# Kernel optimization log

Measured on AMD Instinct MI355X. Metric: run time of the kernel, lower is better.

## Reference

```python
import jax, jax.numpy as jnp
import numpy as np

NUM_HEADS = 12


def setup_inputs() -> dict:
    key = jax.random.key(0)
    k1, k2, k3 = jax.random.split(key, 3)
    B, S, D = 2, 2048, 768
    x = jax.random.normal(k1, (B, S, D), dtype=jnp.float32)
    # torch Linear init: normal(std=0.002) weights, zero bias; stored as [in, out]
    W_qkv = jax.random.normal(k2, (D, 3 * D), dtype=jnp.float32) * 0.002
    b_qkv = jnp.zeros((3 * D,), dtype=jnp.float32)
    W_vw = jax.random.normal(k3, (D, D), dtype=jnp.float32) * 0.002
    b_vw = jnp.zeros((D,), dtype=jnp.float32)
    mask = jnp.ones((B, S), dtype=jnp.int32)  # padding mask, all valid
    return {"x": x, "W_qkv": W_qkv, "b_qkv": b_qkv, "W_vw": W_vw, "b_vw": b_vw, "mask": mask}


def reference(x, W_qkv, b_qkv, W_vw, b_vw, mask):
    B, S, D = x.shape
    H = NUM_HEADS
    Dh = D // H
    qkv = (x @ W_qkv + b_qkv).reshape(B, S, 3, H, Dh)
    q, k, v = qkv[:, :, 0], qkv[:, :, 1], qkv[:, :, 2]
    # [B, H, S, S] attention scores (full matrix, as in original)
    w = jnp.einsum('bshd,bzhd->bhsz', q, k)
    w = w / jnp.sqrt(jnp.asarray(Dh, dtype=x.dtype))  # scale=True
    # log-mask trick: padding mask [B,1,1,S] * causal tril [1,1,S,S]
    causal = jnp.tril(jnp.ones((S, S), dtype=x.dtype))
    wholemask = mask.astype(x.dtype)[:, None, None, :] * causal[None, None]
    w = w + jnp.log(wholemask)
    w = jax.nn.softmax(w, axis=-1)
    vw = jnp.einsum('bhsz,bzhd->bshd', w, v).reshape(B, S, D)
    return vw @ W_vw + b_vw
```

## Files before the change

kernel.cpp:

```cpp
#include <hip/hip_runtime.h>
#include <hip/hip_bf16.h>
#include <cmath>
#include <cstddef>

#define B_    2
#define S_    2048
#define D_    768
#define H_    12
#define DH_   64
#define NQKV_ 2304

typedef __attribute__((ext_vector_type(8))) short  short8;
typedef __attribute__((ext_vector_type(4))) short  short4v;
typedef __attribute__((ext_vector_type(4))) float  floatx4;

__device__ __forceinline__ unsigned short f2bf(float f) {
    union { __hip_bfloat16 h; unsigned short u; } cv;
    cv.h = __float2bfloat16(f);
    return cv.u;
}

__device__ __forceinline__ void stage16(const unsigned short* g, unsigned short* ldsbase, int lane) {
#if __has_builtin(__builtin_amdgcn_global_load_lds)
    __builtin_amdgcn_global_load_lds(
        (const __attribute__((address_space(1))) unsigned int*)g,
        (__attribute__((address_space(3))) unsigned int*)ldsbase, 16, 0, 0);
#else
    *(short8*)(ldsbase + lane * 8) = *(const short8*)g;
#endif
}

__global__ void cvt_x_kernel(const float* __restrict__ x, unsigned short* __restrict__ xb)
{
    int i = (blockIdx.x * 256 + threadIdx.x) * 8;
    float4 a = *(const float4*)(x + i);
    float4 b = *(const float4*)(x + i + 4);
    short8 v;
    v[0] = (short)f2bf(a.x); v[1] = (short)f2bf(a.y);
    v[2] = (short)f2bf(a.z); v[3] = (short)f2bf(a.w);
    v[4] = (short)f2bf(b.x); v[5] = (short)f2bf(b.y);
    v[6] = (short)f2bf(b.z); v[7] = (short)f2bf(b.w);
    *(short8*)(xb + i) = v;
}

__global__ void cvt_w_kernel(const float* __restrict__ Wq, const float* __restrict__ Wv,
                             unsigned short* __restrict__ WqT, unsigned short* __restrict__ WvT)
{
    const int z = blockIdx.z;
    const int N = z ? D_ : NQKV_;
    if ((int)blockIdx.x * 32 >= N) return;
    const float* W = z ? Wv : Wq;
    unsigned short* WT = z ? WvT : WqT;

    __shared__ float t[32][33];
    const int tx = threadIdx.x, ty = threadIdx.y;
    const int n0 = blockIdx.x * 32, k0 = blockIdx.y * 32;
    #pragma unroll
    for (int i = 0; i < 4; ++i)
        t[ty + i * 8][tx] = W[(size_t)(k0 + ty + i * 8) * N + n0 + tx];
    __syncthreads();
    #pragma unroll
    for (int i = 0; i < 4; ++i)
        WT[(size_t)(n0 + ty + i * 8) * 768 + k0 + tx] = f2bf(t[tx][ty + i * 8]);
}

__global__ void vt_kernel(const unsigned short* __restrict__ V, unsigned short* __restrict__ VT)
{
    __shared__ unsigned short t[64][72];
    const int bh = blockIdx.x, s0 = blockIdx.y * 64;
    const unsigned short* src = V + ((size_t)bh * S_ + s0) * DH_;
    const int r = threadIdx.x >> 3, c = (threadIdx.x & 7) * 8;
    #pragma unroll
    for (int it = 0; it < 2; ++it)
        *(short8*)&t[r + it * 32][c] = *(const short8*)(src + (size_t)(r + it * 32) * DH_ + c);
    __syncthreads();
    #pragma unroll
    for (int it = 0; it < 2; ++it) {
        int d = r + it * 32;
        short8 v;
        #pragma unroll
        for (int i = 0; i < 8; ++i) v[i] = (short)t[c + i][d];
        *(short8*)(VT + ((size_t)bh * DH_ + d) * S_ + s0 + c) = v;
    }
}

__global__ __launch_bounds__(256, 2)
void mm_qkv_kernel(const unsigned short* __restrict__ A, const unsigned short* __restrict__ BT,
                   const float* __restrict__ bias,
                   unsigned short* __restrict__ Qo, unsigned short* __restrict__ Ko,
                   unsigned short* __restrict__ Vo)
{
    __shared__ unsigned short As[128][32];
    __shared__ unsigned short Bs[128][32];
    const int tid = threadIdx.x;
    const int wid = tid >> 6, lane = tid & 63;
    const int q = lane >> 4, ln = lane & 15;
    const int wm = (wid & 1) * 64, wn = (wid >> 1) * 64;
    const int m0 = blockIdx.y * 128, n0 = blockIdx.x * 128;
    const int lrow = wid * 16 + (lane >> 2);
    const int lcol = (lane & 3) * 8;
    const unsigned short* Ag = A  + (size_t)(m0 + lrow) * 768 + lcol;
    const unsigned short* Bg = BT + (size_t)(n0 + lrow) * 768 + lcol;

    floatx4 acc[4][4] = {};
    for (int k0 = 0; k0 < 768; k0 += 32) {
        __syncthreads();
        stage16(Ag + k0,            &As[wid * 16][0],      lane);
        stage16(Ag + k0 + 64 * 768, &As[64 + wid * 16][0], lane);
        stage16(Bg + k0,            &Bs[wid * 16][0],      lane);
        stage16(Bg + k0 + 64 * 768, &Bs[64 + wid * 16][0], lane);
        __syncthreads();
        short8 af[4], bf[4];
        #pragma unroll
        for (int mt = 0; mt < 4; ++mt) af[mt] = *(const short8*)&As[wm + mt * 16 + ln][q * 8];
        #pragma unroll
        for (int nt = 0; nt < 4; ++nt) bf[nt] = *(const short8*)&Bs[wn + nt * 16 + ln][q * 8];
        #pragma unroll
        for (int mt = 0; mt < 4; ++mt)
            #pragma unroll
            for (int nt = 0; nt < 4; ++nt)
                acc[mt][nt] = __builtin_amdgcn_mfma_f32_16x16x32_bf16(af[mt], bf[nt], acc[mt][nt], 0, 0, 0);
    }

    const int t = n0 / 768;
    unsigned short* __restrict__ dst = (t == 0) ? Qo : ((t == 1) ? Ko : Vo);
    const float qscale = (t == 0) ? 0.18033688011112042f : 1.0f;
    const int colb = n0 - t * 768 + wn;
    float bv[4];
    #pragma unroll
    for (int nt = 0; nt < 4; ++nt) bv[nt] = bias[n0 + wn + nt * 16 + ln];
    #pragma unroll
    for (int mt = 0; mt < 4; ++mt)
        #pragma unroll
        for (int r = 0; r < 4; ++r) {
            int row = m0 + wm + mt * 16 + q * 4 + r;
            int bb = row >> 11, s = row & 2047;
            #pragma unroll
            for (int nt = 0; nt < 4; ++nt) {
                int col = colb + nt * 16 + ln;
                int h = col >> 6, d = col & 63;
                dst[((size_t)(bb * H_ + h) * S_ + s) * DH_ + d] = f2bf((acc[mt][nt][r] + bv[nt]) * qscale);
            }
        }
}

__global__ __launch_bounds__(256, 2)
void flash9_kernel(const unsigned short* __restrict__ Qg, const unsigned short* __restrict__ Kg,
                   const unsigned short* __restrict__ VTg, const int* __restrict__ mask,
                   unsigned short* __restrict__ VW)
{
    __shared__ unsigned short Pl[4][32][40];
    __shared__ float Ol[32][68];
    __shared__ float li_s[4][32];

    const int tid = threadIdx.x;
    const int wid = tid >> 6, lane = tid & 63;
    const int q = lane >> 4, ln = lane & 15;
    const int bh = blockIdx.x % 24;
    const int qt = 63 - blockIdx.x / 24;
    const int b = bh / H_, h = bh % H_;
    const int r0 = qt * 32;

    const unsigned short* Qb = Qg  + (size_t)bh * S_ * DH_;
    const unsigned short* Kb = Kg  + (size_t)bh * S_ * DH_;
    const unsigned short* Vt = VTg + (size_t)bh * DH_ * S_;
    const int* mb = mask + b * S_;

    short8 qf[2][2];
    #pragma unroll
    for (int rt = 0; rt < 2; ++rt)
        #pragma unroll
        for (int kk = 0; kk < 2; ++kk)
            qf[rt][kk] = *(const short8*)(Qb + (size_t)(r0 + rt * 16 + ln) * DH_ + kk * 32 + q * 8);

    floatx4 o[2][4] = {};
    float li[2] = {};
    const int T = qt + 1;

    for (int t = wid; t < T; t += 4) {
        const int z0 = t * 32;

        short8 kf[2][2];
        #pragma unroll
        for (int zt = 0; zt < 2; ++zt)
            #pragma unroll
            for (int kk = 0; kk < 2; ++kk)
                kf[zt][kk] = *(const short8*)(Kb + (size_t)(z0 + zt * 16 + ln) * DH_ + kk * 32 + q * 8);

        short8 vb[4];
        #pragma unroll
        for (int dt = 0; dt < 4; ++dt)
            vb[dt] = *(const short8*)(Vt + (size_t)(dt * 16 + ln) * S_ + z0 + q * 8);

        const int mi = mb[z0 + (lane & 31)];

        floatx4 s[2][2] = {};
        __builtin_amdgcn_s_setprio(1);
        #pragma unroll
        for (int zt = 0; zt < 2; ++zt)
            #pragma unroll
            for (int rt = 0; rt < 2; ++rt) {
                s[zt][rt] = __builtin_amdgcn_mfma_f32_16x16x32_bf16(kf[zt][0], qf[rt][0], s[zt][rt], 0, 0, 0);
                s[zt][rt] = __builtin_amdgcn_mfma_f32_16x16x32_bf16(kf[zt][1], qf[rt][1], s[zt][rt], 0, 0, 0);
            }
        __builtin_amdgcn_s_setprio(0);

        const bool diag = (z0 + 31 > r0);
        if (__all(mi != 0) && !diag) {
            #pragma unroll
            for (int zt = 0; zt < 2; ++zt)
                #pragma unroll
                for (int rt = 0; rt < 2; ++rt) {
                    float p0 = exp2f(s[zt][rt][0]);
                    float p1 = exp2f(s[zt][rt][1]);
                    float p2 = exp2f(s[zt][rt][2]);
                    float p3 = exp2f(s[zt][rt][3]);
                    li[rt] += (p0 + p1) + (p2 + p3);
                    short4v pk;
                    pk[0] = (short)f2bf(p0); pk[1] = (short)f2bf(p1);
                    pk[2] = (short)f2bf(p2); pk[3] = (short)f2bf(p3);
                    *(short4v*)&Pl[wid][rt * 16 + ln][zt * 16 + q * 4] = pk;
                }
        } else {
            const int4 mA = *(const int4*)&mb[z0 + q * 4];
            const int4 mB = *(const int4*)&mb[z0 + 16 + q * 4];
            int ma[2][4];
            ma[0][0] = mA.x; ma[0][1] = mA.y; ma[0][2] = mA.z; ma[0][3] = mA.w;
            ma[1][0] = mB.x; ma[1][1] = mB.y; ma[1][2] = mB.z; ma[1][3] = mB.w;
            #pragma unroll
            for (int zt = 0; zt < 2; ++zt)
                #pragma unroll
                for (int rt = 0; rt < 2; ++rt) {
                    const int zb = z0 + zt * 16 + q * 4;
                    const int r  = r0 + rt * 16 + ln;
                    float p[4];
                    #pragma unroll
                    for (int rr = 0; rr < 4; ++rr) {
                        p[rr] = exp2f(s[zt][rt][rr]);
                        if (!ma[zt][rr] || (zb + rr > r)) p[rr] = 0.0f;
                    }
                    li[rt] += (p[0] + p[1]) + (p[2] + p[3]);
                    short4v pk;
                    pk[0] = (short)f2bf(p[0]); pk[1] = (short)f2bf(p[1]);
                    pk[2] = (short)f2bf(p[2]); pk[3] = (short)f2bf(p[3]);
                    *(short4v*)&Pl[wid][rt * 16 + ln][zt * 16 + q * 4] = pk;
                }
        }

        #pragma unroll
        for (int mt = 0; mt < 2; ++mt) {
            short8 a = *(const short8*)&Pl[wid][mt * 16 + ln][q * 8];
            __builtin_amdgcn_s_setprio(1);
            #pragma unroll
            for (int dt = 0; dt < 4; ++dt)
                o[mt][dt] = __builtin_amdgcn_mfma_f32_16x16x32_bf16(a, vb[dt], o[mt][dt], 0, 0, 0);
            __builtin_amdgcn_s_setprio(0);
        }
    }

    #pragma unroll
    for (int rt = 0; rt < 2; ++rt) {
        float v = li[rt];
        v += __shfl_xor(v, 16);
        v += __shfl_xor(v, 32);
        li[rt] = v;
    }
    if (lane < 16) {
        li_s[wid][lane]      = li[0];
        li_s[wid][16 + lane] = li[1];
    }

    #pragma unroll
    for (int w = 0; w < 4; ++w) {
        if (wid == w) {
            #pragma unroll
            for (int mt = 0; mt < 2; ++mt)
                #pragma unroll
                for (int r = 0; r < 4; ++r) {
                    int row = mt * 16 + q * 4 + r;
                    #pragma unroll
                    for (int dt = 0; dt < 4; ++dt) {
                        if (w == 0) Ol[row][dt * 16 + ln]  = o[mt][dt][r];
                        else        Ol[row][dt * 16 + ln] += o[mt][dt][r];
                    }
                }
        }
        __syncthreads();
    }

    {
        int row = tid >> 3, c = (tid & 7) * 8;
        float inv = 1.0f / (li_s[0][row] + li_s[1][row] + li_s[2][row] + li_s[3][row]);
        short8 ov;
        #pragma unroll
        for (int i = 0; i < 8; ++i) ov[i] = (short)f2bf(Ol[row][c + i] * inv);
        *(short8*)(VW + ((size_t)b * S_ + r0 + row) * D_ + h * DH_ + c) = ov;
    }
}

__global__ __launch_bounds__(256, 2)
void mm_proj_kernel(const unsigned short* __restrict__ A, const unsigned short* __restrict__ BT,
                    const float* __restrict__ bias, float* __restrict__ C)
{
    __shared__ unsigned short As[128][32];
    __shared__ unsigned short Bs[64][32];
    const int tid = threadIdx.x;
    const int wid = tid >> 6, lane = tid & 63;
    const int q = lane >> 4, ln = lane & 15;
    const int wm = (wid & 1) * 64, wn = (wid >> 1) * 32;
    const int m0 = blockIdx.y * 128, n0 = blockIdx.x * 64;
    const int lrow = wid * 16 + (lane >> 2);
    const int lcol = (lane & 3) * 8;
    const unsigned short* Ag = A  + (size_t)(m0 + lrow) * 768 + lcol;
    const unsigned short* Bg = BT + (size_t)(n0 + lrow) * 768 + lcol;

    floatx4 acc[4][2] = {};
    for (int k0 = 0; k0 < 768; k0 += 32) {
        __syncthreads();
        stage16(Ag + k0,            &As[wid * 16][0],      lane);
        stage16(Ag + k0 + 64 * 768, &As[64 + wid * 16][0], lane);
        stage16(Bg + k0,            &Bs[wid * 16][0],      lane);
        __syncthreads();
        short8 af[4], bf[2];
        #pragma unroll
        for (int mt = 0; mt < 4; ++mt) af[mt] = *(const short8*)&As[wm + mt * 16 + ln][q * 8];
        #pragma unroll
        for (int nt = 0; nt < 2; ++nt) bf[nt] = *(const short8*)&Bs[wn + nt * 16 + ln][q * 8];
        #pragma unroll
        for (int mt = 0; mt < 4; ++mt)
            #pragma unroll
            for (int nt = 0; nt < 2; ++nt)
                acc[mt][nt] = __builtin_amdgcn_mfma_f32_16x16x32_bf16(af[mt], bf[nt], acc[mt][nt], 0, 0, 0);
    }

    float bv[2];
    #pragma unroll
    for (int nt = 0; nt < 2; ++nt) bv[nt] = bias[n0 + wn + nt * 16 + ln];
    #pragma unroll
    for (int mt = 0; mt < 4; ++mt)
        #pragma unroll
        for (int r = 0; r < 4; ++r) {
            size_t row = (size_t)m0 + wm + mt * 16 + q * 4 + r;
            #pragma unroll
            for (int nt = 0; nt < 2; ++nt)
                C[row * D_ + n0 + wn + nt * 16 + ln] = acc[mt][nt][r] + bv[nt];
        }
}

extern "C" void kernel_launch(void* const* d_in, const int* in_sizes, int n_in,
                              void* d_out, int out_size, void* d_ws, size_t ws_size,
                              hipStream_t stream)
{
    (void)in_sizes; (void)n_in; (void)out_size; (void)ws_size;
    const float* x    = (const float*)d_in[0];
    const float* Wqkv = (const float*)d_in[1];
    const float* bqkv = (const float*)d_in[2];
    const float* Wvw  = (const float*)d_in[3];
    const float* bvw  = (const float*)d_in[4];
    const int*   mask = (const int*)d_in[5];
    float* out = (float*)d_out;

    const size_t XN  = (size_t)B_ * S_ * D_;
    unsigned short* ws  = (unsigned short*)d_ws;
    unsigned short* xb  = ws;
    unsigned short* WqT = xb  + XN;
    unsigned short* WvT = WqT + (size_t)NQKV_ * D_;
    unsigned short* Qb  = WvT + (size_t)D_ * D_;
    unsigned short* Kb  = Qb + XN;
    unsigned short* Vb  = Kb + XN;
    unsigned short* VbT = Vb + XN;
    unsigned short* VW  = VbT + XN;

    cvt_x_kernel<<<dim3(XN / (256 * 8)), 256, 0, stream>>>(x, xb);
    cvt_w_kernel<<<dim3(NQKV_ / 32, D_ / 32, 2), dim3(32, 8), 0, stream>>>(Wqkv, Wvw, WqT, WvT);
    mm_qkv_kernel<<<dim3(NQKV_ / 128, (B_ * S_) / 128), 256, 0, stream>>>(xb, WqT, bqkv, Qb, Kb, Vb);
    vt_kernel<<<dim3(B_ * H_, S_ / 64), 256, 0, stream>>>(Vb, VbT);
    flash9_kernel<<<dim3(24 * 64), 256, 0, stream>>>(Qb, Kb, VbT, mask, VW);
    mm_proj_kernel<<<dim3(D_ / 64, (B_ * S_) / 128), 256, 0, stream>>>(VW, WvT, bvw, out);
}
```

Baseline: 179.9 us.

## Software-pipeline PV MFMA one tile behind QK and softmax in flash kernel

Double-buffers the per-wave P tile in LDS and defers each tile's P·V MFMA to the next iteration, so it runs alongside the next tile's QK^T MFMA and exp work. V loads are moved to the deferred step, and a tail step after the loop handles the last tile. The aim is to hide LDS write-to-read latency and give the scheduler independent MFMA work to interleave with the transcendental ops. In exchange it doubles P's LDS footprint and raises register pressure.

```diff
diff --git a/kernel.cpp b/kernel.cpp
--- a/kernel.cpp
+++ b/kernel.cpp
@@ -145,11 +145,11 @@
 }
 
 __global__ __launch_bounds__(256, 2)
-void flash9_kernel(const unsigned short* __restrict__ Qg, const unsigned short* __restrict__ Kg,
-                   const unsigned short* __restrict__ VTg, const int* __restrict__ mask,
-                   unsigned short* __restrict__ VW)
-{
-    __shared__ unsigned short Pl[4][32][40];
+void flash10_kernel(const unsigned short* __restrict__ Qg, const unsigned short* __restrict__ Kg,
+                    const unsigned short* __restrict__ VTg, const int* __restrict__ mask,
+                    unsigned short* __restrict__ VW)
+{
+    __shared__ unsigned short Pl[4][2][32][40];
     __shared__ float Ol[32][68];
     __shared__ float li_s[4][32];
 
@@ -176,6 +176,8 @@
     floatx4 o[2][4] = {};
     float li[2] = {};
     const int T = qt + 1;
+    int par = 0;
+    int tprev = -1;
 
     for (int t = wid; t < T; t += 4) {
         const int z0 = t * 32;
@@ -187,12 +189,24 @@
             for (int kk = 0; kk < 2; ++kk)
                 kf[zt][kk] = *(const short8*)(Kb + (size_t)(z0 + zt * 16 + ln) * DH_ + kk * 32 + q * 8);
 
-        short8 vb[4];
-        #pragma unroll
-        for (int dt = 0; dt < 4; ++dt)
-            vb[dt] = *(const short8*)(Vt + (size_t)(dt * 16 + ln) * S_ + z0 + q * 8);
-
         const int mi = mb[z0 + (lane & 31)];
+
+        if (tprev >= 0) {
+            const int zp = tprev * 32;
+            short8 vb[4];
+            #pragma unroll
+            for (int dt = 0; dt < 4; ++dt)
+                vb[dt] = *(const short8*)(Vt + (size_t)(dt * 16 + ln) * S_ + zp + q * 8);
+            #pragma unroll
+            for (int mt = 0; mt < 2; ++mt) {
+                short8 a = *(const short8*)&Pl[wid][par ^ 1][mt * 16 + ln][q * 8];
+                __builtin_amdgcn_s_setprio(1);
+                #pragma unroll
+                for (int dt = 0; dt < 4; ++dt)
+                    o[mt][dt] = __builtin_amdgcn_mfma_f32_16x16x32_bf16(a, vb[dt], o[mt][dt], 0, 0, 0);
+                __builtin_amdgcn_s_setprio(0);
+            }
+        }
 
         floatx4 s[2][2] = {};
         __builtin_amdgcn_s_setprio(1);
@@ -219,7 +233,7 @@
                     short4v pk;
                     pk[0] = (short)f2bf(p0); pk[1] = (short)f2bf(p1);
                     pk[2] = (short)f2bf(p2); pk[3] = (short)f2bf(p3);
-                    *(short4v*)&Pl[wid][rt * 16 + ln][zt * 16 + q * 4] = pk;
+                    *(short4v*)&Pl[wid][par][rt * 16 + ln][zt * 16 + q * 4] = pk;
                 }
         } else {
             const int4 mA = *(const int4*)&mb[z0 + q * 4];
@@ -243,13 +257,23 @@
                     short4v pk;
                     pk[0] = (short)f2bf(p[0]); pk[1] = (short)f2bf(p[1]);
                     pk[2] = (short)f2bf(p[2]); pk[3] = (short)f2bf(p[3]);
-                    *(short4v*)&Pl[wid][rt * 16 + ln][zt * 16 + q * 4] = pk;
+                    *(short4v*)&Pl[wid][par][rt * 16 + ln][zt * 16 + q * 4] = pk;
                 }
         }
 
+        tprev = t;
+        par ^= 1;
+    }
+
+    if (tprev >= 0) {
+        const int zp = tprev * 32;
+        short8 vb[4];
+        #pragma unroll
+        for (int dt = 0; dt < 4; ++dt)
+            vb[dt] = *(const short8*)(Vt + (size_t)(dt * 16 + ln) * S_ + zp + q * 8);
         #pragma unroll
         for (int mt = 0; mt < 2; ++mt) {
-            short8 a = *(const short8*)&Pl[wid][mt * 16 + ln][q * 8];
+            short8 a = *(const short8*)&Pl[wid][par ^ 1][mt * 16 + ln][q * 8];
             __builtin_amdgcn_s_setprio(1);
             #pragma unroll
             for (int dt = 0; dt < 4; ++dt)
@@ -375,6 +399,6 @@
     cvt_w_kernel<<<dim3(NQKV_ / 32, D_ / 32, 2), dim3(32, 8), 0, stream>>>(Wqkv, Wvw, WqT, WvT);
     mm_qkv_kernel<<<dim3(NQKV_ / 128, (B_ * S_) / 128), 256, 0, stream>>>(xb, WqT, bqkv, Qb, Kb, Vb);
     vt_kernel<<<dim3(B_ * H_, S_ / 64), 256, 0, stream>>>(Vb, VbT);
-    flash9_kernel<<<dim3(24 * 64), 256, 0, stream>>>(Qb, Kb, VbT, mask, VW);
+    flash10_kernel<<<dim3(24 * 64), 256, 0, stream>>>(Qb, Kb, VbT, mask, VW);
     mm_proj_kernel<<<dim3(D_ / 64, (B_ * S_) / 128), 256, 0, stream>>>(VW, WvT, bvw, out);
 }
```

Result: no change. 178.2 us (-0.9%).

## Restructure flash attention so each wave owns query rows with shared LDS K/V tiles

Applied to the files above, without the earlier changes.

Each block now covers 128 query rows, and each of its four waves owns 32 of them, instead of four waves splitting the key range of one 32-row tile. K and V tiles are staged once per block into double-buffered, XOR-swizzled LDS via global_load_lds and shared by all waves. Because every wave now holds a complete softmax row, the cross-wave LDS reduction of O and row sums is removed. The costs are a __syncthreads per key tile, idle waves on the causal triangle (waves skip tiles past their diagonal), and far fewer blocks (384 vs 1536), which cuts parallelism and can leave load imbalance.

```diff
diff --git a/kernel.cpp b/kernel.cpp
--- a/kernel.cpp
+++ b/kernel.cpp
@@ -145,54 +145,75 @@
 }
 
 __global__ __launch_bounds__(256, 2)
-void flash9_kernel(const unsigned short* __restrict__ Qg, const unsigned short* __restrict__ Kg,
-                   const unsigned short* __restrict__ VTg, const int* __restrict__ mask,
-                   unsigned short* __restrict__ VW)
-{
+void flash12_kernel(const unsigned short* __restrict__ Qg, const unsigned short* __restrict__ Kg,
+                    const unsigned short* __restrict__ VTg, const int* __restrict__ mask,
+                    unsigned short* __restrict__ VW)
+{
+    __shared__ unsigned short Ks[2][32][64];
+    __shared__ unsigned short Vs[2][64][32];
     __shared__ unsigned short Pl[4][32][40];
-    __shared__ float Ol[32][68];
-    __shared__ float li_s[4][32];
 
     const int tid = threadIdx.x;
     const int wid = tid >> 6, lane = tid & 63;
     const int q = lane >> 4, ln = lane & 15;
     const int bh = blockIdx.x % 24;
-    const int qt = 63 - blockIdx.x / 24;
+    const int j  = 15 - blockIdx.x / 24;
     const int b = bh / H_, h = bh % H_;
-    const int r0 = qt * 32;
+    const int r0 = j * 128;
+    const int r0w = r0 + wid * 32;
+    const int T = 4 * j + 4;
+    const int Lw = 4 * j + wid + 1;
 
     const unsigned short* Qb = Qg  + (size_t)bh * S_ * DH_;
     const unsigned short* Kb = Kg  + (size_t)bh * S_ * DH_;
     const unsigned short* Vt = VTg + (size_t)bh * DH_ * S_;
     const int* mb = mask + b * S_;
 
+    const int krow = wid * 8 + (lane >> 3);
+    const int kslt = ((lane & 7) ^ (lane >> 3)) * 8;
+    const int vrow = wid * 16 + (lane >> 2);
+    const int vslt = (((lane & 3) ^ ((lane >> 2) & 3))) * 8;
+
     short8 qf[2][2];
     #pragma unroll
     for (int rt = 0; rt < 2; ++rt)
         #pragma unroll
         for (int kk = 0; kk < 2; ++kk)
-            qf[rt][kk] = *(const short8*)(Qb + (size_t)(r0 + rt * 16 + ln) * DH_ + kk * 32 + q * 8);
+            qf[rt][kk] = *(const short8*)(Qb + (size_t)(r0w + rt * 16 + ln) * DH_ + kk * 32 + q * 8);
 
     floatx4 o[2][4] = {};
     float li[2] = {};
-    const int T = qt + 1;
-
-    for (int t = wid; t < T; t += 4) {
+
+    stage16(Kb + (size_t)(krow) * DH_ + kslt,  &Ks[0][wid * 8][0],  lane);
+    stage16(Vt + (size_t)(vrow) * S_  + vslt,  &Vs[0][wid * 16][0], lane);
+
+    for (int t = 0; t < T; ++t) {
+        __syncthreads();
+
         const int z0 = t * 32;
+        const int mi = mb[z0 + (lane & 31)];
+
+        if (t + 1 < T) {
+            const int z1 = z0 + 32;
+            const int nb = (t + 1) & 1;
+            stage16(Kb + (size_t)(z1 + krow) * DH_ + kslt, &Ks[nb][wid * 8][0],  lane);
+            stage16(Vt + (size_t)(vrow) * S_ + z1 + vslt,  &Vs[nb][wid * 16][0], lane);
+        }
+
+        if (t >= Lw) continue;
+        const int cb = t & 1;
 
         short8 kf[2][2];
         #pragma unroll
         for (int zt = 0; zt < 2; ++zt)
             #pragma unroll
             for (int kk = 0; kk < 2; ++kk)
-                kf[zt][kk] = *(const short8*)(Kb + (size_t)(z0 + zt * 16 + ln) * DH_ + kk * 32 + q * 8);
+                kf[zt][kk] = *(const short8*)&Ks[cb][zt * 16 + ln][(((kk * 4 + q) ^ (ln & 7)) * 8)];
 
         short8 vb[4];
         #pragma unroll
         for (int dt = 0; dt < 4; ++dt)
-            vb[dt] = *(const short8*)(Vt + (size_t)(dt * 16 + ln) * S_ + z0 + q * 8);
-
-        const int mi = mb[z0 + (lane & 31)];
+            vb[dt] = *(const short8*)&Vs[cb][dt * 16 + ln][((q ^ (ln & 3)) * 8)];
 
         floatx4 s[2][2] = {};
         __builtin_amdgcn_s_setprio(1);
@@ -205,7 +226,7 @@
             }
         __builtin_amdgcn_s_setprio(0);
 
-        const bool diag = (z0 + 31 > r0);
+        const bool diag = (t == Lw - 1);
         if (__all(mi != 0) && !diag) {
             #pragma unroll
             for (int zt = 0; zt < 2; ++zt)
@@ -232,7 +253,7 @@
                 #pragma unroll
                 for (int rt = 0; rt < 2; ++rt) {
                     const int zb = z0 + zt * 16 + q * 4;
-                    const int r  = r0 + rt * 16 + ln;
+                    const int r  = r0w + rt * 16 + ln;
                     float p[4];
                     #pragma unroll
                     for (int rr = 0; rr < 4; ++rr) {
@@ -265,36 +286,21 @@
         v += __shfl_xor(v, 32);
         li[rt] = v;
     }
-    if (lane < 16) {
-        li_s[wid][lane]      = li[0];
-        li_s[wid][16 + lane] = li[1];
-    }
-
-    #pragma unroll
-    for (int w = 0; w < 4; ++w) {
-        if (wid == w) {
-            #pragma unroll
-            for (int mt = 0; mt < 2; ++mt)
-                #pragma unroll
-                for (int r = 0; r < 4; ++r) {
-                    int row = mt * 16 + q * 4 + r;
-                    #pragma unroll
-                    for (int dt = 0; dt < 4; ++dt) {
-                        if (w == 0) Ol[row][dt * 16 + ln]  = o[mt][dt][r];
-                        else        Ol[row][dt * 16 + ln] += o[mt][dt][r];
-                    }
-                }
-        }
-        __syncthreads();
-    }
-
-    {
-        int row = tid >> 3, c = (tid & 7) * 8;
-        float inv = 1.0f / (li_s[0][row] + li_s[1][row] + li_s[2][row] + li_s[3][row]);
-        short8 ov;
-        #pragma unroll
-        for (int i = 0; i < 8; ++i) ov[i] = (short)f2bf(Ol[row][c + i] * inv);
-        *(short8*)(VW + ((size_t)b * S_ + r0 + row) * D_ + h * DH_ + c) = ov;
+
+    #pragma unroll
+    for (int mt = 0; mt < 2; ++mt) {
+        float inv[4];
+        #pragma unroll
+        for (int rr = 0; rr < 4; ++rr)
+            inv[rr] = 1.0f / __shfl(li[mt], q * 4 + rr);
+        #pragma unroll
+        for (int rr = 0; rr < 4; ++rr) {
+            int srow = r0w + mt * 16 + q * 4 + rr;
+            unsigned short* dst = VW + ((size_t)b * S_ + srow) * D_ + h * DH_ + ln;
+            #pragma unroll
+            for (int dt = 0; dt < 4; ++dt)
+                dst[dt * 16] = f2bf(o[mt][dt][rr] * inv[rr]);
+        }
     }
 }
 
@@ -375,6 +381,6 @@
     cvt_w_kernel<<<dim3(NQKV_ / 32, D_ / 32, 2), dim3(32, 8), 0, stream>>>(Wqkv, Wvw, WqT, WvT);
     mm_qkv_kernel<<<dim3(NQKV_ / 128, (B_ * S_) / 128), 256, 0, stream>>>(xb, WqT, bqkv, Qb, Kb, Vb);
     vt_kernel<<<dim3(B_ * H_, S_ / 64), 256, 0, stream>>>(Vb, VbT);
-    flash9_kernel<<<dim3(24 * 64), 256, 0, stream>>>(Qb, Kb, VbT, mask, VW);
+    flash12_kernel<<<dim3(24 * 16), 256, 0, stream>>>(Qb, Kb, VbT, mask, VW);
     mm_proj_kernel<<<dim3(D_ / 64, (B_ * S_) / 128), 256, 0, stream>>>(VW, WvT, bvw, out);
 }
```

New measurement: 190.2 us. 5.7% more time.
